# Performance work log

Measured on AMD Instinct MI355X. Metric: run time of the kernel, lower is better.

## Reference

```python
import jax, jax.numpy as jnp
import numpy as np

BN_EPS = 1e-5

def conv1x1(x, w, b):
    # x: [B,C,H,W], w: [O,C], b: [O] -> [B,O,H,W]
    return jnp.einsum('bchw,oc->bohw', x, w) + b[None, :, None, None]

def maxpool2x2(x):
    B, C, H, W = x.shape
    return x.reshape(B, C, H // 2, 2, W // 2, 2).max(axis=(3, 5))

def setup_inputs() -> dict:
    key = jax.random.key(0)
    ks = jax.random.split(key, 12)
    B, C, Ci, H, W = 8, 256, 128, 64, 64
    s_in = 1.0 / np.sqrt(C)
    s_mid = 1.0 / np.sqrt(Ci)
    return {
        'x': jax.random.normal(ks[0], (B, C, H, W), jnp.float32),
        'y': jax.random.normal(ks[1], (B, C, H, W), jnp.float32),
        'theta_w': jax.random.normal(ks[2], (Ci, C), jnp.float32) * s_in,
        'theta_b': jax.random.normal(ks[3], (Ci,), jnp.float32) * s_in,
        'phi_w': jax.random.normal(ks[4], (Ci, C), jnp.float32) * s_in,
        'phi_b': jax.random.normal(ks[5], (Ci,), jnp.float32) * s_in,
        'g_w': jax.random.normal(ks[6], (Ci, C), jnp.float32) * s_in,
        'g_b': jax.random.normal(ks[7], (Ci,), jnp.float32) * s_in,
        'w_w': jax.random.normal(ks[8], (C, Ci), jnp.float32) * s_mid,
        'w_b': jax.random.normal(ks[9], (C,), jnp.float32) * s_mid,
        'bn_gamma': jax.random.normal(ks[10], (C,), jnp.float32),
        'bn_beta': jax.random.normal(ks[11], (C,), jnp.float32),
    }

def reference(x, y, theta_w, theta_b, phi_w, phi_b, g_w, g_b, w_w, w_b, bn_gamma, bn_beta):
    B, C, H, W = x.shape
    Ci = theta_w.shape[0]
    # Q: [B, N, Ci] from x (no subsample)
    theta_x = conv1x1(x, theta_w, theta_b).reshape(B, Ci, H * W).transpose(0, 2, 1)
    # K: [B, Ci, M] and V: [B, M, Ci] from y (2x2 maxpool subsample)
    phi_x = maxpool2x2(conv1x1(y, phi_w, phi_b)).reshape(B, Ci, -1)
    g_x = maxpool2x2(conv1x1(y, g_w, g_b)).reshape(B, Ci, -1).transpose(0, 2, 1)
    # unscaled dot-product attention, softmax over keys
    f = jnp.einsum('bnc,bcm->bnm', theta_x, phi_x)        # [B, N, M]
    attn = jax.nn.softmax(f, axis=-1)
    out = jnp.einsum('bnm,bmc->bnc', attn, g_x)            # [B, N, Ci]
    out = out.transpose(0, 2, 1).reshape(B, Ci, H, W)
    # W projection (1x1 conv) + BatchNorm (batch statistics, training mode)
    wy = conv1x1(out, w_w, w_b)
    mean = wy.mean(axis=(0, 2, 3))
    var = wy.var(axis=(0, 2, 3))
    wy = (wy - mean[None, :, None, None]) * jax.lax.rsqrt(var[None, :, None, None] + BN_EPS)
    wy = wy * bn_gamma[None, :, None, None] + bn_beta[None, :, None, None]
    return wy + x
```

## Files before the change

kernel.cpp:

```cpp
#include <hip/hip_runtime.h>

#define B_  8
#define C_  256
#define CI_ 128
#define N_  4096
#define M_  1024

typedef unsigned short u16;
typedef __attribute__((ext_vector_type(8))) short short8;
typedef __attribute__((ext_vector_type(4))) float f32x4;

__device__ __forceinline__ u16 f2bf(float f) {
    unsigned int u = __float_as_uint(f);
    u += 0x7fffu + ((u >> 16) & 1u);
    return (u16)(u >> 16);
}
__device__ __forceinline__ float bf2f(u16 h) {
    return __uint_as_float(((unsigned int)h) << 16);
}

__global__ __launch_bounds__(256) void prep_w_kernel(
    const float* __restrict__ tw, const float* __restrict__ pw,
    const float* __restrict__ gw, const float* __restrict__ ww,
    u16* __restrict__ out_h, u16* __restrict__ out_l)
{
    int t = blockIdx.x * 256 + threadIdx.x;
    int wsel = t >> 12, idx = t & 4095;
    int lane = idx & 63;
    const float* src; int F, Cdim;
    if (wsel == 3)      { src = ww; F = 16; Cdim = 128; }
    else if (wsel == 0) { src = tw; F = 8;  Cdim = 256; }
    else if (wsel == 1) { src = pw; F = 8;  Cdim = 256; }
    else                { src = gw; F = 8;  Cdim = 256; }
    int fk = idx >> 6;
    int ks = fk / F, f = fk - ks * F;
    int o = f * 16 + (lane & 15);
    int c = ks * 32 + (lane >> 4) * 8;
    const float* s = src + (size_t)o * Cdim + c;
    float4 v0 = *(const float4*)s;
    float4 v1 = *(const float4*)(s + 4);
    float vv[8] = {v0.x, v0.y, v0.z, v0.w, v1.x, v1.y, v1.z, v1.w};
    short8 hv, lv;
    #pragma unroll
    for (int j = 0; j < 8; ++j) {
        u16 h = f2bf(vv[j]);
        hv[j] = (short)h;
        lv[j] = (short)f2bf(vv[j] - bf2f(h));
    }
    size_t oo = (size_t)wsel * 32768 + (size_t)idx * 8;
    *(short8*)&out_h[oo] = hv;
    *(short8*)&out_l[oo] = lv;
}

__global__ __launch_bounds__(256) void qconv_kernel(
    const float* __restrict__ x,
    const u16* __restrict__ Bfh, const u16* __restrict__ Bfl,
    const float* __restrict__ bias,
    u16* __restrict__ qhi, u16* __restrict__ qlo)
{
    const int tid = threadIdx.x;
    const int wave = tid >> 6, lane = tid & 63;
    const int tx = lane & 15, quad = lane >> 4;
    const int ot = blockIdx.y, b = blockIdx.z;
    const int nw = blockIdx.x * 64 + wave * 16;

    f32x4 acc[4];
    #pragma unroll
    for (int i = 0; i < 4; ++i) acc[i] = (f32x4){0.f, 0.f, 0.f, 0.f};

    #pragma unroll
    for (int ks = 0; ks < 8; ++ks) {
        const size_t cbase = ((size_t)b * C_ + ks * 32 + quad * 8) * N_ + nw + tx;
        float a[8];
        #pragma unroll
        for (int j = 0; j < 8; ++j) a[j] = x[cbase + (size_t)j * N_];
        short8 ah, al;
        #pragma unroll
        for (int j = 0; j < 8; ++j) {
            u16 h = f2bf(a[j]);
            ah[j] = (short)h;
            al[j] = (short)f2bf(a[j] - bf2f(h));
        }
        #pragma unroll
        for (int fi = 0; fi < 4; ++fi) {
            int f = ot * 4 + fi;
            size_t bo = ((size_t)(ks * 8 + f) * 64 + lane) * 8;
            short8 bh = *(const short8*)&Bfh[bo];
            short8 bl = *(const short8*)&Bfl[bo];
            acc[fi] = __builtin_amdgcn_mfma_f32_16x16x32_bf16(ah, bh, acc[fi], 0, 0, 0);
            acc[fi] = __builtin_amdgcn_mfma_f32_16x16x32_bf16(ah, bl, acc[fi], 0, 0, 0);
            acc[fi] = __builtin_amdgcn_mfma_f32_16x16x32_bf16(al, bh, acc[fi], 0, 0, 0);
        }
    }

    #pragma unroll
    for (int fi = 0; fi < 4; ++fi) {
        int f = ot * 4 + fi;
        float bv = bias[f * 16 + tx];
        #pragma unroll
        for (int r = 0; r < 4; ++r) {
            float v = acc[fi][r] + bv;
            size_t addr = ((size_t)(b * N_ + nw + quad * 4 + r)) * CI_ + f * 16 + tx;
            u16 h = f2bf(v);
            qhi[addr] = h;
            qlo[addr] = f2bf(v - bf2f(h));
        }
    }
}

__global__ __launch_bounds__(256) void kvconv_kernel(
    const float* __restrict__ y,
    const u16* __restrict__ PfH, const u16* __restrict__ PfL,
    const u16* __restrict__ GfH, const u16* __restrict__ GfL,
    const float* __restrict__ phib, const float* __restrict__ gb,
    u16* __restrict__ khi, u16* __restrict__ klo, u16* __restrict__ vf)
{
    const int tid = threadIdx.x;
    const int w = tid >> 6, lane = tid & 63;
    const int tx = lane & 15, quad = lane >> 4;
    const int t = blockIdx.x, ot = blockIdx.y, b = blockIdx.z;

    const size_t nA = (size_t)t * 128 + w * 16 + tx;
    const size_t nB = nA + 64;

    f32x4 accP[2][4], accG[2][4];
    #pragma unroll
    for (int i = 0; i < 2; ++i)
        #pragma unroll
        for (int j = 0; j < 4; ++j) {
            accP[i][j] = (f32x4){0.f, 0.f, 0.f, 0.f};
            accG[i][j] = (f32x4){0.f, 0.f, 0.f, 0.f};
        }

    #pragma unroll
    for (int ks = 0; ks < 8; ++ks) {
        const size_t cbase = ((size_t)b * C_ + ks * 32 + quad * 8) * N_;
        float a0[8], a1[8];
        #pragma unroll
        for (int j = 0; j < 8; ++j) {
            a0[j] = y[cbase + (size_t)j * N_ + nA];
            a1[j] = y[cbase + (size_t)j * N_ + nB];
        }
        short8 ah0, al0, ah1, al1;
        #pragma unroll
        for (int j = 0; j < 8; ++j) {
            u16 h = f2bf(a0[j]); ah0[j] = (short)h; al0[j] = (short)f2bf(a0[j] - bf2f(h));
            h = f2bf(a1[j]);     ah1[j] = (short)h; al1[j] = (short)f2bf(a1[j] - bf2f(h));
        }
        #pragma unroll
        for (int of = 0; of < 4; ++of) {
            int f = ot * 4 + of;
            size_t bo = ((size_t)(ks * 8 + f) * 64 + lane) * 8;
            short8 ph = *(const short8*)&PfH[bo];
            short8 pl = *(const short8*)&PfL[bo];
            short8 gh = *(const short8*)&GfH[bo];
            short8 gl = *(const short8*)&GfL[bo];
            accP[0][of] = __builtin_amdgcn_mfma_f32_16x16x32_bf16(ah0, ph, accP[0][of], 0, 0, 0);
            accP[0][of] = __builtin_amdgcn_mfma_f32_16x16x32_bf16(ah0, pl, accP[0][of], 0, 0, 0);
            accP[0][of] = __builtin_amdgcn_mfma_f32_16x16x32_bf16(al0, ph, accP[0][of], 0, 0, 0);
            accP[1][of] = __builtin_amdgcn_mfma_f32_16x16x32_bf16(ah1, ph, accP[1][of], 0, 0, 0);
            accP[1][of] = __builtin_amdgcn_mfma_f32_16x16x32_bf16(ah1, pl, accP[1][of], 0, 0, 0);
            accP[1][of] = __builtin_amdgcn_mfma_f32_16x16x32_bf16(al1, ph, accP[1][of], 0, 0, 0);
            accG[0][of] = __builtin_amdgcn_mfma_f32_16x16x32_bf16(ah0, gh, accG[0][of], 0, 0, 0);
            accG[0][of] = __builtin_amdgcn_mfma_f32_16x16x32_bf16(ah0, gl, accG[0][of], 0, 0, 0);
            accG[0][of] = __builtin_amdgcn_mfma_f32_16x16x32_bf16(al0, gh, accG[0][of], 0, 0, 0);
            accG[1][of] = __builtin_amdgcn_mfma_f32_16x16x32_bf16(ah1, gh, accG[1][of], 0, 0, 0);
            accG[1][of] = __builtin_amdgcn_mfma_f32_16x16x32_bf16(ah1, gl, accG[1][of], 0, 0, 0);
            accG[1][of] = __builtin_amdgcn_mfma_f32_16x16x32_bf16(al1, gh, accG[1][of], 0, 0, 0);
        }
    }

    #pragma unroll
    for (int of = 0; of < 4; ++of) {
        int ci = (ot * 4 + of) * 16 + tx;
        float pb = phib[ci], gbv = gb[ci];
        #pragma unroll
        for (int j = 0; j < 2; ++j) {
            float vP = fmaxf(fmaxf(accP[0][of][2 * j], accP[0][of][2 * j + 1]),
                             fmaxf(accP[1][of][2 * j], accP[1][of][2 * j + 1])) + pb;
            float vG = fmaxf(fmaxf(accG[0][of][2 * j], accG[0][of][2 * j + 1]),
                             fmaxf(accG[1][of][2 * j], accG[1][of][2 * j + 1])) + gbv;
            int mm = 8 * w + 2 * quad + j;
            int fragK = (mm >> 4) * 4 + (ci >> 5);
            int laneK = (((ci & 31) >> 3) << 4) + (mm & 15);
            size_t ka = (((size_t)(b * 32 + t) * 8 + fragK) * 64 + laneK) * 8 + (ci & 7);
            u16 h = f2bf(vP);
            khi[ka] = h;
            klo[ka] = f2bf(vP - bf2f(h));
            int fragV = ci >> 4;
            size_t va = (((size_t)(b * 32 + t) * 8 + fragV) * 64 + w * 16 + tx) * 8 + (2 * quad + j);
            vf[va] = f2bf(vG);
        }
    }
}

__global__ __launch_bounds__(256, 4) void attn_kernel(
    const u16* __restrict__ Qhi, const u16* __restrict__ Qlo,
    const u16* __restrict__ Kfh, const u16* __restrict__ Kfl,
    const u16* __restrict__ Vf,
    float* __restrict__ OP0, float* __restrict__ OP1,
    float* __restrict__ L0, float* __restrict__ L1)
{
    __shared__ __align__(16) u16 kh_sh[4096];
    __shared__ __align__(16) u16 kl_sh[4096];
    __shared__ __align__(16) u16 vf_sh[4096];
    __shared__ __align__(16) u16 p_sh[4][16 * 40];

    const int tid = threadIdx.x;
    const int wave = tid >> 6, lane = tid & 63;
    const int tx = lane & 15, quad = lane >> 4;
    const int half = blockIdx.y, b = blockIdx.z;
    const int q0 = blockIdx.x * 64 + wave * 16;
    const float FM = 48.f;

    float* OP = half ? OP1 : OP0;
    float* Lp = half ? L1 : L0;

    short8 qh[4], ql[4];
    {
        const u16* qp  = Qhi + ((size_t)b * N_ + q0 + tx) * CI_ + quad * 8;
        const u16* qp2 = Qlo + ((size_t)b * N_ + q0 + tx) * CI_ + quad * 8;
        #pragma unroll
        for (int ks = 0; ks < 4; ++ks) {
            qh[ks] = *(const short8*)&qp[ks * 32];
            ql[ks] = *(const short8*)&qp2[ks * 32];
        }
    }

    f32x4 acc[8];
    #pragma unroll
    for (int f = 0; f < 8; ++f) acc[f] = (f32x4){0.f, 0.f, 0.f, 0.f};
    float lrun[4] = {0.f, 0.f, 0.f, 0.f};

    const u16* Khb = Kfh + (size_t)b * 32 * 4096 + (size_t)half * 16 * 4096;
    const u16* Klb = Kfl + (size_t)b * 32 * 4096 + (size_t)half * 16 * 4096;
    const u16* Vb  = Vf  + (size_t)b * 32 * 4096 + (size_t)half * 16 * 4096;

    for (int ch = 0; ch < 16; ++ch) {
        __syncthreads();
        #pragma unroll
        for (int rp = 0; rp < 2; ++rp) {
            int idx = (tid + 256 * rp) * 8;
            *(short8*)&kh_sh[idx] = *(const short8*)&Khb[ch * 4096 + idx];
            *(short8*)&kl_sh[idx] = *(const short8*)&Klb[ch * 4096 + idx];
            *(short8*)&vf_sh[idx] = *(const short8*)&Vb [ch * 4096 + idx];
        }
        __syncthreads();

        f32x4 s0 = (f32x4){0.f, 0.f, 0.f, 0.f};
        f32x4 s1 = (f32x4){0.f, 0.f, 0.f, 0.f};
        #pragma unroll
        for (int ks = 0; ks < 4; ++ks) {
            short8 bh0 = *(const short8*)&kh_sh[ks * 512 + lane * 8];
            short8 bl0 = *(const short8*)&kl_sh[ks * 512 + lane * 8];
            short8 bh1 = *(const short8*)&kh_sh[(4 + ks) * 512 + lane * 8];
            short8 bl1 = *(const short8*)&kl_sh[(4 + ks) * 512 + lane * 8];
            s0 = __builtin_amdgcn_mfma_f32_16x16x32_bf16(qh[ks], bh0, s0, 0, 0, 0);
            s0 = __builtin_amdgcn_mfma_f32_16x16x32_bf16(qh[ks], bl0, s0, 0, 0, 0);
            s0 = __builtin_amdgcn_mfma_f32_16x16x32_bf16(ql[ks], bh0, s0, 0, 0, 0);
            s1 = __builtin_amdgcn_mfma_f32_16x16x32_bf16(qh[ks], bh1, s1, 0, 0, 0);
            s1 = __builtin_amdgcn_mfma_f32_16x16x32_bf16(qh[ks], bl1, s1, 0, 0, 0);
            s1 = __builtin_amdgcn_mfma_f32_16x16x32_bf16(ql[ks], bh1, s1, 0, 0, 0);
        }

        u16* pw_ = p_sh[wave];
        #pragma unroll
        for (int r = 0; r < 4; ++r) {
            float p0 = __expf(s0[r] - FM);
            float p1 = __expf(s1[r] - FM);
            lrun[r] += p0 + p1;
            pw_[(4 * quad + r) * 40 + tx]      = f2bf(p0);
            pw_[(4 * quad + r) * 40 + 16 + tx] = f2bf(p1);
        }
        asm volatile("s_waitcnt lgkmcnt(0)" ::: "memory");
        short8 pf = *(const short8*)&pw_[tx * 40 + quad * 8];

        #pragma unroll
        for (int f = 0; f < 8; ++f) {
            short8 vb = *(const short8*)&vf_sh[f * 512 + lane * 8];
            acc[f] = __builtin_amdgcn_mfma_f32_16x16x32_bf16(pf, vb, acc[f], 0, 0, 0);
        }
    }

    #pragma unroll
    for (int d = 1; d < 16; d <<= 1) {
        #pragma unroll
        for (int r = 0; r < 4; ++r) lrun[r] += __shfl_xor(lrun[r], d);
    }
    if (tx == 0) {
        #pragma unroll
        for (int r = 0; r < 4; ++r)
            Lp[(size_t)b * N_ + q0 + 4 * quad + r] = lrun[r];
    }
    float* Ob = OP + ((size_t)b * N_ + q0) * CI_;
    #pragma unroll
    for (int f = 0; f < 8; ++f) {
        #pragma unroll
        for (int r = 0; r < 4; ++r)
            Ob[(size_t)(4 * quad + r) * CI_ + f * 16 + tx] = acc[f][r];
    }
}

__global__ __launch_bounds__(256) void attn_merge_kernel(
    const float* __restrict__ OP0, const float* __restrict__ OP1,
    const float* __restrict__ L0, const float* __restrict__ L1,
    u16* __restrict__ Oh)
{
    int gid = blockIdx.x * 256 + threadIdx.x;
    size_t base = (size_t)gid * 4;
    int row = (int)(base >> 7);
    float inv = 1.f / (L0[row] + L1[row]);
    float4 a = *(const float4*)&OP0[base];
    float4 c = *(const float4*)&OP1[base];
    u16 o0 = f2bf((a.x + c.x) * inv);
    u16 o1 = f2bf((a.y + c.y) * inv);
    u16 o2 = f2bf((a.z + c.z) * inv);
    u16 o3 = f2bf((a.w + c.w) * inv);
    *(uint2*)&Oh[base] = make_uint2((unsigned)o0 | ((unsigned)o1 << 16),
                                    (unsigned)o2 | ((unsigned)o3 << 16));
}

__global__ __launch_bounds__(256) void wconv_mfma_kernel(
    const u16* __restrict__ Bh,
    const u16* __restrict__ Afh, const u16* __restrict__ Afl,
    const float* __restrict__ bias, float* __restrict__ wy,
    float* __restrict__ part)
{
    const int tid = threadIdx.x;
    const int wave = tid >> 6, lane = tid & 63;
    const int tx = lane & 15, quad = lane >> 4;
    const int id = blockIdx.x;
    const int xcd = id & 7;
    const int s = id >> 3;
    const int ot = s & 1;
    const int gnt = (s >> 1) * 8 + xcd;
    const int b = gnt >> 7;
    const int n0 = (gnt & 127) * 32;
    const int of0 = ot * 8 + wave * 2, of1 = of0 + 1;

    short8 wah[4][2], wal[4][2];
    #pragma unroll
    for (int ks = 0; ks < 4; ++ks) {
        #pragma unroll
        for (int ff = 0; ff < 2; ++ff) {
            size_t aa = ((size_t)(ks * 16 + of0 + ff) * 64 + lane) * 8;
            wah[ks][ff] = *(const short8*)&Afh[aa];
            wal[ks][ff] = *(const short8*)&Afl[aa];
        }
    }

    f32x4 acc[2][2];
    #pragma unroll
    for (int i = 0; i < 2; ++i)
        #pragma unroll
        for (int j = 0; j < 2; ++j) acc[i][j] = (f32x4){0.f, 0.f, 0.f, 0.f};

    #pragma unroll
    for (int ks = 0; ks < 4; ++ks) {
        short8 bh[2];
        #pragma unroll
        for (int nf = 0; nf < 2; ++nf) {
            size_t ba = ((size_t)(b * N_ + n0 + nf * 16 + tx)) * CI_ + ks * 32 + quad * 8;
            bh[nf] = *(const short8*)&Bh[ba];
        }
        #pragma unroll
        for (int ff = 0; ff < 2; ++ff) {
            #pragma unroll
            for (int nf = 0; nf < 2; ++nf) {
                acc[ff][nf] = __builtin_amdgcn_mfma_f32_16x16x32_bf16(wah[ks][ff], bh[nf], acc[ff][nf], 0, 0, 0);
                acc[ff][nf] = __builtin_amdgcn_mfma_f32_16x16x32_bf16(wal[ks][ff], bh[nf], acc[ff][nf], 0, 0, 0);
            }
        }
    }

    #pragma unroll
    for (int ff = 0; ff < 2; ++ff) {
        int fg = ff ? of1 : of0;
        #pragma unroll
        for (int r = 0; r < 4; ++r) {
            int o = fg * 16 + quad * 4 + r;
            float bo = bias[o];
            float ps = 0.f, pss = 0.f;
            #pragma unroll
            for (int nf = 0; nf < 2; ++nf) {
                float v = acc[ff][nf][r] + bo;
                wy[((size_t)b * C_ + o) * N_ + n0 + nf * 16 + tx] = v;
                ps += v; pss += v * v;
            }
            #pragma unroll
            for (int d = 1; d < 16; d <<= 1) {
                ps  += __shfl_xor(ps, d);
                pss += __shfl_xor(pss, d);
            }
            if (tx == 0) {
                part[(size_t)o * 1024 + gnt]          = ps;
                part[262144 + (size_t)o * 1024 + gnt] = pss;
            }
        }
    }
}

__global__ __launch_bounds__(256) void bn_reduce_kernel(
    const float* __restrict__ part, float* __restrict__ sums)
{
    int w = blockIdx.x * 4 + (threadIdx.x >> 6);
    int lane = threadIdx.x & 63;
    int p = w >> 8, o = w & 255;
    const float* src = part + (size_t)p * 262144 + (size_t)o * 1024;
    float s = 0.f;
    #pragma unroll
    for (int j = 0; j < 16; ++j) s += src[j * 64 + lane];
    #pragma unroll
    for (int d = 1; d < 64; d <<= 1) s += __shfl_xor(s, d);
    if (lane == 0) sums[p * 256 + o] = s;
}

__global__ __launch_bounds__(256) void bn_final_kernel(
    const float* __restrict__ wy, const float* __restrict__ x,
    const float* __restrict__ gsum, const float* __restrict__ gsumsq,
    const float* __restrict__ gamma, const float* __restrict__ beta,
    float* __restrict__ out)
{
    int idx = blockIdx.x * 256 + threadIdx.x;
    size_t base = (size_t)idx * 4;
    int o = (int)((base >> 12) & 255);
    float4 wv = *(const float4*)&wy[base];
    float4 xv = *(const float4*)&x[base];
    const float invc = 1.f / 32768.f;
    float mean = gsum[o] * invc;
    float var  = gsumsq[o] * invc - mean * mean;
    float sc = gamma[o] * rsqrtf(var + 1e-5f);
    float sh = beta[o] - mean * sc;
    float4 r;
    r.x = wv.x * sc + sh + xv.x;
    r.y = wv.y * sc + sh + xv.y;
    r.z = wv.z * sc + sh + xv.z;
    r.w = wv.w * sc + sh + xv.w;
    *(float4*)&out[base] = r;
}

extern "C" void kernel_launch(void* const* d_in, const int* in_sizes, int n_in,
                              void* d_out, int out_size, void* d_ws, size_t ws_size,
                              hipStream_t stream) {
    (void)in_sizes; (void)n_in; (void)out_size; (void)ws_size;
    const float* x       = (const float*)d_in[0];
    const float* y       = (const float*)d_in[1];
    const float* theta_w = (const float*)d_in[2];
    const float* theta_b = (const float*)d_in[3];
    const float* phi_w   = (const float*)d_in[4];
    const float* phi_b   = (const float*)d_in[5];
    const float* g_w     = (const float*)d_in[6];
    const float* g_b     = (const float*)d_in[7];
    const float* w_w     = (const float*)d_in[8];
    const float* w_b     = (const float*)d_in[9];
    const float* bn_g    = (const float*)d_in[10];
    const float* bn_b    = (const float*)d_in[11];
    float* out = (float*)d_out;

    float* ws = (float*)d_ws;
    float* OP0  = ws;
    float* OP1  = ws + 4194304;
    float* WY   = ws;
    float* L0   = ws + 8388608;
    float* L1   = ws + 8421376;
    u16*   Qhi  = (u16*)(ws + 8454144);
    u16*   Qlo  = (u16*)(ws + 10551296);
    float* PART = ws + 8454144;
    u16*   Kfh  = (u16*)(ws + 12648448);
    u16*   Kfl  = (u16*)(ws + 13172736);
    u16*   Vfp  = (u16*)(ws + 13697024);
    u16*   Oh   = (u16*)(ws + 14221312);
    u16*   Wfh  = (u16*)(ws + 16318464);
    u16*   Wfl  = (u16*)(ws + 16384000);
    float* SUMS = ws + 16449536;

    prep_w_kernel<<<64, 256, 0, stream>>>(theta_w, phi_w, g_w, w_w, Wfh, Wfl);

    qconv_kernel<<<dim3(64, 2, 8), 256, 0, stream>>>(
        x, Wfh, Wfl, theta_b, Qhi, Qlo);
    kvconv_kernel<<<dim3(32, 2, 8), 256, 0, stream>>>(
        y, Wfh + 32768, Wfl + 32768, Wfh + 65536, Wfl + 65536,
        phi_b, g_b, Kfh, Kfl, Vfp);

    attn_kernel<<<dim3(64, 2, 8), 256, 0, stream>>>(
        Qhi, Qlo, Kfh, Kfl, Vfp, OP0, OP1, L0, L1);
    attn_merge_kernel<<<4096, 256, 0, stream>>>(OP0, OP1, L0, L1, Oh);

    wconv_mfma_kernel<<<2048, 256, 0, stream>>>(
        Oh, Wfh + 98304, Wfl + 98304, w_b, WY, PART);
    bn_reduce_kernel<<<128, 256, 0, stream>>>(PART, SUMS);
    bn_final_kernel<<<8192, 256, 0, stream>>>(WY, x, SUMS, SUMS + 256, bn_g, bn_b, out);
}
```

Baseline: 243.5 us.

## Replace split-bf16 MFMA emulation with single fp16 MFMA across all stages

Every GEMM previously built near-fp32 precision from three (or two) bf16 MFMAs using hi/lo splits. It now runs one fp16 MFMA and stores Q, K, attention partials, merged O and the W-projection output in fp16. This cuts MFMA count roughly threefold and halves the intermediate memory traffic. The attention kernel also prefetches the next K/V chunk into registers and normalizes each partial before merging. The risk is lower accuracy: fp16 has limited range for unscaled logits and for the pre-BN activations.

```diff
diff --git a/kernel.cpp b/kernel.cpp
--- a/kernel.cpp
+++ b/kernel.cpp
@@ -7,7 +7,10 @@
 #define M_  1024
 
 typedef unsigned short u16;
+typedef _Float16 f16;
 typedef __attribute__((ext_vector_type(8))) short short8;
+typedef __attribute__((ext_vector_type(8))) _Float16 half8;
+typedef __attribute__((ext_vector_type(4))) _Float16 half4;
 typedef __attribute__((ext_vector_type(4))) float f32x4;
 
 __device__ __forceinline__ u16 f2bf(float f) {
@@ -22,7 +25,7 @@
 __global__ __launch_bounds__(256) void prep_w_kernel(
     const float* __restrict__ tw, const float* __restrict__ pw,
     const float* __restrict__ gw, const float* __restrict__ ww,
-    u16* __restrict__ out_h, u16* __restrict__ out_l)
+    f16* __restrict__ out_h)
 {
     int t = blockIdx.x * 256 + threadIdx.x;
     int wsel = t >> 12, idx = t & 4095;
@@ -39,24 +42,17 @@
     const float* s = src + (size_t)o * Cdim + c;
     float4 v0 = *(const float4*)s;
     float4 v1 = *(const float4*)(s + 4);
-    float vv[8] = {v0.x, v0.y, v0.z, v0.w, v1.x, v1.y, v1.z, v1.w};
-    short8 hv, lv;
-    #pragma unroll
-    for (int j = 0; j < 8; ++j) {
-        u16 h = f2bf(vv[j]);
-        hv[j] = (short)h;
-        lv[j] = (short)f2bf(vv[j] - bf2f(h));
-    }
+    half8 hv;
+    hv[0] = (f16)v0.x; hv[1] = (f16)v0.y; hv[2] = (f16)v0.z; hv[3] = (f16)v0.w;
+    hv[4] = (f16)v1.x; hv[5] = (f16)v1.y; hv[6] = (f16)v1.z; hv[7] = (f16)v1.w;
     size_t oo = (size_t)wsel * 32768 + (size_t)idx * 8;
-    *(short8*)&out_h[oo] = hv;
-    *(short8*)&out_l[oo] = lv;
+    *(half8*)&out_h[oo] = hv;
 }
 
 __global__ __launch_bounds__(256) void qconv_kernel(
     const float* __restrict__ x,
-    const u16* __restrict__ Bfh, const u16* __restrict__ Bfl,
-    const float* __restrict__ bias,
-    u16* __restrict__ qhi, u16* __restrict__ qlo)
+    const f16* __restrict__ Bfh, const float* __restrict__ bias,
+    f16* __restrict__ qh_out)
 {
     const int tid = threadIdx.x;
     const int wave = tid >> 6, lane = tid & 63;
@@ -74,22 +70,15 @@
         float a[8];
         #pragma unroll
         for (int j = 0; j < 8; ++j) a[j] = x[cbase + (size_t)j * N_];
-        short8 ah, al;
-        #pragma unroll
-        for (int j = 0; j < 8; ++j) {
-            u16 h = f2bf(a[j]);
-            ah[j] = (short)h;
-            al[j] = (short)f2bf(a[j] - bf2f(h));
-        }
+        half8 ah;
+        #pragma unroll
+        for (int j = 0; j < 8; ++j) ah[j] = (f16)a[j];
         #pragma unroll
         for (int fi = 0; fi < 4; ++fi) {
             int f = ot * 4 + fi;
             size_t bo = ((size_t)(ks * 8 + f) * 64 + lane) * 8;
-            short8 bh = *(const short8*)&Bfh[bo];
-            short8 bl = *(const short8*)&Bfl[bo];
-            acc[fi] = __builtin_amdgcn_mfma_f32_16x16x32_bf16(ah, bh, acc[fi], 0, 0, 0);
-            acc[fi] = __builtin_amdgcn_mfma_f32_16x16x32_bf16(ah, bl, acc[fi], 0, 0, 0);
-            acc[fi] = __builtin_amdgcn_mfma_f32_16x16x32_bf16(al, bh, acc[fi], 0, 0, 0);
+            half8 bh = *(const half8*)&Bfh[bo];
+            acc[fi] = __builtin_amdgcn_mfma_f32_16x16x32_f16(ah, bh, acc[fi], 0, 0, 0);
         }
     }
 
@@ -99,21 +88,17 @@
         float bv = bias[f * 16 + tx];
         #pragma unroll
         for (int r = 0; r < 4; ++r) {
-            float v = acc[fi][r] + bv;
             size_t addr = ((size_t)(b * N_ + nw + quad * 4 + r)) * CI_ + f * 16 + tx;
-            u16 h = f2bf(v);
-            qhi[addr] = h;
-            qlo[addr] = f2bf(v - bf2f(h));
+            qh_out[addr] = (f16)(acc[fi][r] + bv);
         }
     }
 }
 
 __global__ __launch_bounds__(256) void kvconv_kernel(
     const float* __restrict__ y,
-    const u16* __restrict__ PfH, const u16* __restrict__ PfL,
-    const u16* __restrict__ GfH, const u16* __restrict__ GfL,
+    const f16* __restrict__ PfH, const f16* __restrict__ GfH,
     const float* __restrict__ phib, const float* __restrict__ gb,
-    u16* __restrict__ khi, u16* __restrict__ klo, u16* __restrict__ vf)
+    f16* __restrict__ khi, u16* __restrict__ vf)
 {
     const int tid = threadIdx.x;
     const int w = tid >> 6, lane = tid & 63;
@@ -141,32 +126,22 @@
             a0[j] = y[cbase + (size_t)j * N_ + nA];
             a1[j] = y[cbase + (size_t)j * N_ + nB];
         }
-        short8 ah0, al0, ah1, al1;
+        half8 ah0, ah1;
         #pragma unroll
         for (int j = 0; j < 8; ++j) {
-            u16 h = f2bf(a0[j]); ah0[j] = (short)h; al0[j] = (short)f2bf(a0[j] - bf2f(h));
-            h = f2bf(a1[j]);     ah1[j] = (short)h; al1[j] = (short)f2bf(a1[j] - bf2f(h));
+            ah0[j] = (f16)a0[j];
+            ah1[j] = (f16)a1[j];
         }
         #pragma unroll
         for (int of = 0; of < 4; ++of) {
             int f = ot * 4 + of;
             size_t bo = ((size_t)(ks * 8 + f) * 64 + lane) * 8;
-            short8 ph = *(const short8*)&PfH[bo];
-            short8 pl = *(const short8*)&PfL[bo];
-            short8 gh = *(const short8*)&GfH[bo];
-            short8 gl = *(const short8*)&GfL[bo];
-            accP[0][of] = __builtin_amdgcn_mfma_f32_16x16x32_bf16(ah0, ph, accP[0][of], 0, 0, 0);
-            accP[0][of] = __builtin_amdgcn_mfma_f32_16x16x32_bf16(ah0, pl, accP[0][of], 0, 0, 0);
-            accP[0][of] = __builtin_amdgcn_mfma_f32_16x16x32_bf16(al0, ph, accP[0][of], 0, 0, 0);
-            accP[1][of] = __builtin_amdgcn_mfma_f32_16x16x32_bf16(ah1, ph, accP[1][of], 0, 0, 0);
-            accP[1][of] = __builtin_amdgcn_mfma_f32_16x16x32_bf16(ah1, pl, accP[1][of], 0, 0, 0);
-            accP[1][of] = __builtin_amdgcn_mfma_f32_16x16x32_bf16(al1, ph, accP[1][of], 0, 0, 0);
-            accG[0][of] = __builtin_amdgcn_mfma_f32_16x16x32_bf16(ah0, gh, accG[0][of], 0, 0, 0);
-            accG[0][of] = __builtin_amdgcn_mfma_f32_16x16x32_bf16(ah0, gl, accG[0][of], 0, 0, 0);
-            accG[0][of] = __builtin_amdgcn_mfma_f32_16x16x32_bf16(al0, gh, accG[0][of], 0, 0, 0);
-            accG[1][of] = __builtin_amdgcn_mfma_f32_16x16x32_bf16(ah1, gh, accG[1][of], 0, 0, 0);
-            accG[1][of] = __builtin_amdgcn_mfma_f32_16x16x32_bf16(ah1, gl, accG[1][of], 0, 0, 0);
-            accG[1][of] = __builtin_amdgcn_mfma_f32_16x16x32_bf16(al1, gh, accG[1][of], 0, 0, 0);
+            half8 ph = *(const half8*)&PfH[bo];
+            half8 gh = *(const half8*)&GfH[bo];
+            accP[0][of] = __builtin_amdgcn_mfma_f32_16x16x32_f16(ah0, ph, accP[0][of], 0, 0, 0);
+            accP[1][of] = __builtin_amdgcn_mfma_f32_16x16x32_f16(ah1, ph, accP[1][of], 0, 0, 0);
+            accG[0][of] = __builtin_amdgcn_mfma_f32_16x16x32_f16(ah0, gh, accG[0][of], 0, 0, 0);
+            accG[1][of] = __builtin_amdgcn_mfma_f32_16x16x32_f16(ah1, gh, accG[1][of], 0, 0, 0);
         }
     }
 
@@ -184,9 +159,7 @@
             int fragK = (mm >> 4) * 4 + (ci >> 5);
             int laneK = (((ci & 31) >> 3) << 4) + (mm & 15);
             size_t ka = (((size_t)(b * 32 + t) * 8 + fragK) * 64 + laneK) * 8 + (ci & 7);
-            u16 h = f2bf(vP);
-            khi[ka] = h;
-            klo[ka] = f2bf(vP - bf2f(h));
+            khi[ka] = (f16)vP;
             int fragV = ci >> 4;
             size_t va = (((size_t)(b * 32 + t) * 8 + fragV) * 64 + w * 16 + tx) * 8 + (2 * quad + j);
             vf[va] = f2bf(vG);
@@ -194,15 +167,11 @@
     }
 }
 
-__global__ __launch_bounds__(256, 4) void attn_kernel(
-    const u16* __restrict__ Qhi, const u16* __restrict__ Qlo,
-    const u16* __restrict__ Kfh, const u16* __restrict__ Kfl,
-    const u16* __restrict__ Vf,
-    float* __restrict__ OP0, float* __restrict__ OP1,
-    float* __restrict__ L0, float* __restrict__ L1)
-{
-    __shared__ __align__(16) u16 kh_sh[4096];
-    __shared__ __align__(16) u16 kl_sh[4096];
+__global__ __launch_bounds__(256) void attn_kernel(
+    const f16* __restrict__ Qh, const f16* __restrict__ Kf,
+    const u16* __restrict__ Vf, f16* __restrict__ OP, float* __restrict__ L)
+{
+    __shared__ __align__(16) f16 kh_sh[4096];
     __shared__ __align__(16) u16 vf_sh[4096];
     __shared__ __align__(16) u16 p_sh[4][16 * 40];
 
@@ -213,18 +182,11 @@
     const int q0 = blockIdx.x * 64 + wave * 16;
     const float FM = 48.f;
 
-    float* OP = half ? OP1 : OP0;
-    float* Lp = half ? L1 : L0;
-
-    short8 qh[4], ql[4];
+    half8 qh[4];
     {
-        const u16* qp  = Qhi + ((size_t)b * N_ + q0 + tx) * CI_ + quad * 8;
-        const u16* qp2 = Qlo + ((size_t)b * N_ + q0 + tx) * CI_ + quad * 8;
-        #pragma unroll
-        for (int ks = 0; ks < 4; ++ks) {
-            qh[ks] = *(const short8*)&qp[ks * 32];
-            ql[ks] = *(const short8*)&qp2[ks * 32];
-        }
+        const f16* qp = Qh + ((size_t)b * N_ + q0 + tx) * CI_ + quad * 8;
+        #pragma unroll
+        for (int ks = 0; ks < 4; ++ks) qh[ks] = *(const half8*)&qp[ks * 32];
     }
 
     f32x4 acc[8];
@@ -232,18 +194,32 @@
     for (int f = 0; f < 8; ++f) acc[f] = (f32x4){0.f, 0.f, 0.f, 0.f};
     float lrun[4] = {0.f, 0.f, 0.f, 0.f};
 
-    const u16* Khb = Kfh + (size_t)b * 32 * 4096 + (size_t)half * 16 * 4096;
-    const u16* Klb = Kfl + (size_t)b * 32 * 4096 + (size_t)half * 16 * 4096;
-    const u16* Vb  = Vf  + (size_t)b * 32 * 4096 + (size_t)half * 16 * 4096;
+    const f16* Khb = Kf + ((size_t)b * 32 + half * 16) * 4096;
+    const u16* Vb  = Vf + ((size_t)b * 32 + half * 16) * 4096;
+
+    half8 rk[2]; short8 rv[2];
+    #pragma unroll
+    for (int rp = 0; rp < 2; ++rp) {
+        int idx = (tid + 256 * rp) * 8;
+        rk[rp] = *(const half8*)&Khb[idx];
+        rv[rp] = *(const short8*)&Vb[idx];
+    }
 
     for (int ch = 0; ch < 16; ++ch) {
         __syncthreads();
         #pragma unroll
         for (int rp = 0; rp < 2; ++rp) {
             int idx = (tid + 256 * rp) * 8;
-            *(short8*)&kh_sh[idx] = *(const short8*)&Khb[ch * 4096 + idx];
-            *(short8*)&kl_sh[idx] = *(const short8*)&Klb[ch * 4096 + idx];
-            *(short8*)&vf_sh[idx] = *(const short8*)&Vb [ch * 4096 + idx];
+            *(half8*)&kh_sh[idx] = rk[rp];
+            *(short8*)&vf_sh[idx] = rv[rp];
+        }
+        if (ch + 1 < 16) {
+            #pragma unroll
+            for (int rp = 0; rp < 2; ++rp) {
+                int idx = (tid + 256 * rp) * 8;
+                rk[rp] = *(const half8*)&Khb[(ch + 1) * 4096 + idx];
+                rv[rp] = *(const short8*)&Vb[(ch + 1) * 4096 + idx];
+            }
         }
         __syncthreads();
 
@@ -251,16 +227,10 @@
         f32x4 s1 = (f32x4){0.f, 0.f, 0.f, 0.f};
         #pragma unroll
         for (int ks = 0; ks < 4; ++ks) {
-            short8 bh0 = *(const short8*)&kh_sh[ks * 512 + lane * 8];
-            short8 bl0 = *(const short8*)&kl_sh[ks * 512 + lane * 8];
-            short8 bh1 = *(const short8*)&kh_sh[(4 + ks) * 512 + lane * 8];
-            short8 bl1 = *(const short8*)&kl_sh[(4 + ks) * 512 + lane * 8];
-            s0 = __builtin_amdgcn_mfma_f32_16x16x32_bf16(qh[ks], bh0, s0, 0, 0, 0);
-            s0 = __builtin_amdgcn_mfma_f32_16x16x32_bf16(qh[ks], bl0, s0, 0, 0, 0);
-            s0 = __builtin_amdgcn_mfma_f32_16x16x32_bf16(ql[ks], bh0, s0, 0, 0, 0);
-            s1 = __builtin_amdgcn_mfma_f32_16x16x32_bf16(qh[ks], bh1, s1, 0, 0, 0);
-            s1 = __builtin_amdgcn_mfma_f32_16x16x32_bf16(qh[ks], bl1, s1, 0, 0, 0);
-            s1 = __builtin_amdgcn_mfma_f32_16x16x32_bf16(ql[ks], bh1, s1, 0, 0, 0);
+            half8 bh0 = *(const half8*)&kh_sh[ks * 512 + lane * 8];
+            half8 bh1 = *(const half8*)&kh_sh[(4 + ks) * 512 + lane * 8];
+            s0 = __builtin_amdgcn_mfma_f32_16x16x32_f16(qh[ks], bh0, s0, 0, 0, 0);
+            s1 = __builtin_amdgcn_mfma_f32_16x16x32_f16(qh[ks], bh1, s1, 0, 0, 0);
         }
 
         u16* pw_ = p_sh[wave];
@@ -290,40 +260,43 @@
     if (tx == 0) {
         #pragma unroll
         for (int r = 0; r < 4; ++r)
-            Lp[(size_t)b * N_ + q0 + 4 * quad + r] = lrun[r];
-    }
-    float* Ob = OP + ((size_t)b * N_ + q0) * CI_;
+            L[(size_t)half * 32768 + b * N_ + q0 + 4 * quad + r] = lrun[r];
+    }
+    float inv[4];
+    #pragma unroll
+    for (int r = 0; r < 4; ++r) inv[r] = 1.f / lrun[r];
+    f16* Ob = OP + ((size_t)half * B_ + b) * N_ * CI_ + (size_t)q0 * CI_;
     #pragma unroll
     for (int f = 0; f < 8; ++f) {
         #pragma unroll
         for (int r = 0; r < 4; ++r)
-            Ob[(size_t)(4 * quad + r) * CI_ + f * 16 + tx] = acc[f][r];
+            Ob[(size_t)(4 * quad + r) * CI_ + f * 16 + tx] = (f16)(acc[f][r] * inv[r]);
     }
 }
 
 __global__ __launch_bounds__(256) void attn_merge_kernel(
-    const float* __restrict__ OP0, const float* __restrict__ OP1,
-    const float* __restrict__ L0, const float* __restrict__ L1,
-    u16* __restrict__ Oh)
+    const f16* __restrict__ OP, const float* __restrict__ L,
+    f16* __restrict__ Oh)
 {
     int gid = blockIdx.x * 256 + threadIdx.x;
     size_t base = (size_t)gid * 4;
     int row = (int)(base >> 7);
-    float inv = 1.f / (L0[row] + L1[row]);
-    float4 a = *(const float4*)&OP0[base];
-    float4 c = *(const float4*)&OP1[base];
-    u16 o0 = f2bf((a.x + c.x) * inv);
-    u16 o1 = f2bf((a.y + c.y) * inv);
-    u16 o2 = f2bf((a.z + c.z) * inv);
-    u16 o3 = f2bf((a.w + c.w) * inv);
-    *(uint2*)&Oh[base] = make_uint2((unsigned)o0 | ((unsigned)o1 << 16),
-                                    (unsigned)o2 | ((unsigned)o3 << 16));
+    float l0 = L[row], l1 = L[32768 + row];
+    float invs = 1.f / (l0 + l1);
+    float w0 = l0 * invs, w1 = l1 * invs;
+    half4 a = *(const half4*)&OP[base];
+    half4 c = *(const half4*)&OP[4194304 + base];
+    half4 o;
+    o[0] = (f16)((float)a[0] * w0 + (float)c[0] * w1);
+    o[1] = (f16)((float)a[1] * w0 + (float)c[1] * w1);
+    o[2] = (f16)((float)a[2] * w0 + (float)c[2] * w1);
+    o[3] = (f16)((float)a[3] * w0 + (float)c[3] * w1);
+    *(half4*)&Oh[base] = o;
 }
 
 __global__ __launch_bounds__(256) void wconv_mfma_kernel(
-    const u16* __restrict__ Bh,
-    const u16* __restrict__ Afh, const u16* __restrict__ Afl,
-    const float* __restrict__ bias, float* __restrict__ wy,
+    const f16* __restrict__ Bh, const f16* __restrict__ Afh,
+    const float* __restrict__ bias, f16* __restrict__ wy,
     float* __restrict__ part)
 {
     const int tid = threadIdx.x;
@@ -338,14 +311,13 @@
     const int n0 = (gnt & 127) * 32;
     const int of0 = ot * 8 + wave * 2, of1 = of0 + 1;
 
-    short8 wah[4][2], wal[4][2];
+    half8 wah[4][2];
     #pragma unroll
     for (int ks = 0; ks < 4; ++ks) {
         #pragma unroll
         for (int ff = 0; ff < 2; ++ff) {
             size_t aa = ((size_t)(ks * 16 + of0 + ff) * 64 + lane) * 8;
-            wah[ks][ff] = *(const short8*)&Afh[aa];
-            wal[ks][ff] = *(const short8*)&Afl[aa];
+            wah[ks][ff] = *(const half8*)&Afh[aa];
         }
     }
 
@@ -357,20 +329,17 @@
 
     #pragma unroll
     for (int ks = 0; ks < 4; ++ks) {
-        short8 bh[2];
+        half8 bh[2];
         #pragma unroll
         for (int nf = 0; nf < 2; ++nf) {
             size_t ba = ((size_t)(b * N_ + n0 + nf * 16 + tx)) * CI_ + ks * 32 + quad * 8;
-            bh[nf] = *(const short8*)&Bh[ba];
-        }
-        #pragma unroll
-        for (int ff = 0; ff < 2; ++ff) {
+            bh[nf] = *(const half8*)&Bh[ba];
+        }
+        #pragma unroll
+        for (int ff = 0; ff < 2; ++ff)
             #pragma unroll
-            for (int nf = 0; nf < 2; ++nf) {
-                acc[ff][nf] = __builtin_amdgcn_mfma_f32_16x16x32_bf16(wah[ks][ff], bh[nf], acc[ff][nf], 0, 0, 0);
-                acc[ff][nf] = __builtin_amdgcn_mfma_f32_16x16x32_bf16(wal[ks][ff], bh[nf], acc[ff][nf], 0, 0, 0);
-            }
-        }
+            for (int nf = 0; nf < 2; ++nf)
+                acc[ff][nf] = __builtin_amdgcn_mfma_f32_16x16x32_f16(wah[ks][ff], bh[nf], acc[ff][nf], 0, 0, 0);
     }
 
     #pragma unroll
@@ -384,7 +353,7 @@
             #pragma unroll
             for (int nf = 0; nf < 2; ++nf) {
                 float v = acc[ff][nf][r] + bo;
-                wy[((size_t)b * C_ + o) * N_ + n0 + nf * 16 + tx] = v;
+                wy[((size_t)b * C_ + o) * N_ + n0 + nf * 16 + tx] = (f16)v;
                 ps += v; pss += v * v;
             }
             #pragma unroll
@@ -416,7 +385,7 @@
 }
 
 __global__ __launch_bounds__(256) void bn_final_kernel(
-    const float* __restrict__ wy, const float* __restrict__ x,
+    const f16* __restrict__ wy, const float* __restrict__ x,
     const float* __restrict__ gsum, const float* __restrict__ gsumsq,
     const float* __restrict__ gamma, const float* __restrict__ beta,
     float* __restrict__ out)
@@ -424,7 +393,7 @@
     int idx = blockIdx.x * 256 + threadIdx.x;
     size_t base = (size_t)idx * 4;
     int o = (int)((base >> 12) & 255);
-    float4 wv = *(const float4*)&wy[base];
+    half4 wv = *(const half4*)&wy[base];
     float4 xv = *(const float4*)&x[base];
     const float invc = 1.f / 32768.f;
     float mean = gsum[o] * invc;
@@ -432,10 +401,10 @@
     float sc = gamma[o] * rsqrtf(var + 1e-5f);
     float sh = beta[o] - mean * sc;
     float4 r;
-    r.x = wv.x * sc + sh + xv.x;
-    r.y = wv.y * sc + sh + xv.y;
-    r.z = wv.z * sc + sh + xv.z;
-    r.w = wv.w * sc + sh + xv.w;
+    r.x = (float)wv[0] * sc + sh + xv.x;
+    r.y = (float)wv[1] * sc + sh + xv.y;
+    r.z = (float)wv[2] * sc + sh + xv.z;
+    r.w = (float)wv[3] * sc + sh + xv.w;
     *(float4*)&out[base] = r;
 }
 
@@ -458,36 +427,27 @@
     float* out = (float*)d_out;
 
     float* ws = (float*)d_ws;
-    float* OP0  = ws;
-    float* OP1  = ws + 4194304;
-    float* WY   = ws;
-    float* L0   = ws + 8388608;
-    float* L1   = ws + 8421376;
-    u16*   Qhi  = (u16*)(ws + 8454144);
-    u16*   Qlo  = (u16*)(ws + 10551296);
-    float* PART = ws + 8454144;
-    u16*   Kfh  = (u16*)(ws + 12648448);
-    u16*   Kfl  = (u16*)(ws + 13172736);
-    u16*   Vfp  = (u16*)(ws + 13697024);
-    u16*   Oh   = (u16*)(ws + 14221312);
-    u16*   Wfh  = (u16*)(ws + 16318464);
-    u16*   Wfl  = (u16*)(ws + 16384000);
-    float* SUMS = ws + 16449536;
-
-    prep_w_kernel<<<64, 256, 0, stream>>>(theta_w, phi_w, g_w, w_w, Wfh, Wfl);
-
-    qconv_kernel<<<dim3(64, 2, 8), 256, 0, stream>>>(
-        x, Wfh, Wfl, theta_b, Qhi, Qlo);
+    f16*   Qh   = (f16*)(ws);
+    f16*   Kf   = (f16*)(ws + 2097152);
+    u16*   Vfp  = (u16*)(ws + 2621440);
+    f16*   OP   = (f16*)(ws + 3145728);
+    float* L    = ws + 7340032;
+    f16*   Oh   = (f16*)(ws + 7405568);
+    f16*   WY   = (f16*)(ws + 9502720);
+    float* PART = ws + 13697024;
+    f16*   Wfh  = (f16*)(ws + 14221312);
+    float* SUMS = ws + 14286848;
+
+    prep_w_kernel<<<64, 256, 0, stream>>>(theta_w, phi_w, g_w, w_w, Wfh);
+
+    qconv_kernel<<<dim3(64, 2, 8), 256, 0, stream>>>(x, Wfh, theta_b, Qh);
     kvconv_kernel<<<dim3(32, 2, 8), 256, 0, stream>>>(
-        y, Wfh + 32768, Wfl + 32768, Wfh + 65536, Wfl + 65536,
-        phi_b, g_b, Kfh, Kfl, Vfp);
-
-    attn_kernel<<<dim3(64, 2, 8), 256, 0, stream>>>(
-        Qhi, Qlo, Kfh, Kfl, Vfp, OP0, OP1, L0, L1);
-    attn_merge_kernel<<<4096, 256, 0, stream>>>(OP0, OP1, L0, L1, Oh);
-
-    wconv_mfma_kernel<<<2048, 256, 0, stream>>>(
-        Oh, Wfh + 98304, Wfl + 98304, w_b, WY, PART);
+        y, Wfh + 32768, Wfh + 65536, phi_b, g_b, Kf, Vfp);
+
+    attn_kernel<<<dim3(64, 2, 8), 256, 0, stream>>>(Qh, Kf, Vfp, OP, L);
+    attn_merge_kernel<<<4096, 256, 0, stream>>>(OP, L, Oh);
+
+    wconv_mfma_kernel<<<2048, 256, 0, stream>>>(Oh, Wfh + 98304, w_b, WY, PART);
     bn_reduce_kernel<<<128, 256, 0, stream>>>(PART, SUMS);
     bn_final_kernel<<<8192, 256, 0, stream>>>(WY, x, SUMS, SUMS + 256, bn_g, bn_b, out);
 }
```

Measured after the change: 213.0 us. -12.5%, faster.
